# Performance work log

Measured on AMD Instinct MI355X. Metric: run time of the kernel, lower is better.

The kernel has to match this reference:

```python
import jax, jax.numpy as jnp
import numpy as np

B, N, C = 16, 4096, 512
H = 8                      # num_heads
HEIGHT = WIDTH = 64        # input_resolution, HEIGHT*WIDTH == N
D = C // H                 # head_dim = 64
SCALE = D ** (-0.25)       # head_dim ** -0.25 (applied to both axial logits)


def setup_inputs() -> dict:
    key = jax.random.key(0)
    k0, k1, k2 = jax.random.split(key, 3)
    return {
        "x": jax.random.normal(k0, (B, N, C), jnp.float32),
        "W_qkv": jax.random.normal(k1, (C, 3 * C), jnp.float32) / np.sqrt(C).astype(np.float32),
        "b_qkv": jnp.zeros((3 * C,), jnp.float32),
        "W_proj": jax.random.normal(k2, (C, C), jnp.float32) / np.sqrt(C).astype(np.float32),
        "b_proj": jnp.zeros((C,), jnp.float32),
    }


def reference(x, W_qkv, b_qkv, W_proj, b_proj):
    Bx, Nx, Cx = x.shape
    # qkv projection -> [3, B, H, height, width, D]
    qkv = (x @ W_qkv + b_qkv).reshape(Bx, Nx, 3, H, D)
    qkv = jnp.transpose(qkv, (2, 0, 3, 1, 4)).reshape(3, Bx, H, HEIGHT, WIDTH, D)
    q, k, v = qkv[0], qkv[1], qkv[2]

    # row attention (channel_merge='concat'): contract over (width, channel)
    a = jnp.einsum('bhiwc,bhjwc->bhij', q, k) * SCALE          # [B,H,height,height]
    a = jax.nn.softmax(a, axis=-1)
    # column attention: contract over (height, channel)
    bm = jnp.einsum('bhtic,bhtjc->bhij', q, k) * SCALE         # [B,H,width,width]
    bm = jax.nn.softmax(bm, axis=-1)

    # coupled combination: (v_perm @ b^T) then a @ (...)
    # tmp[b,h,c,t,u] = sum_w v[b,h,t,w,c] * bm[b,h,u,w]
    tmp = jnp.einsum('bhtwc,bhuw->bhctu', v, bm)               # [B,H,D,height,width]
    out = jnp.einsum('bhij,bhcjw->bhciw', a, tmp)              # [B,H,D,height,width]

    out = out.reshape(Bx, Cx, Nx).transpose(0, 2, 1)           # [B,N,C]
    return out @ W_proj + b_proj
```

## Files before the change

kernel.cpp:

```cpp
#include <hip/hip_runtime.h>
#include <math.h>

#define SCALE_F 0.35355339059327373f

typedef unsigned short u16;
typedef unsigned int   u32;
typedef _Float16 f16;
typedef _Float16 f16x8 __attribute__((ext_vector_type(8)));
typedef float    f32x4 __attribute__((ext_vector_type(4)));

__device__ __forceinline__ u16 f2h(float f) { f16 h = (f16)f; return *(u16*)&h; }
__device__ __forceinline__ float h2f(u16 b) { f16 h = *(f16*)&b; return (float)h; }

__device__ __forceinline__ void glds16(const u16* g, char* l) {
    __builtin_amdgcn_global_load_lds((const __attribute__((address_space(1))) void*)g,
                                     (__attribute__((address_space(3))) void*)l, 16, 0, 0);
}
__device__ __forceinline__ f32x4 mfma16(f16x8 a, f16x8 b, f32x4 c) {
    return __builtin_amdgcn_mfma_f32_16x16x32_f16(a, b, c, 0, 0, 0);
}

__global__ __launch_bounds__(256) void to_f16(
    const float* __restrict__ X, u16* __restrict__ out)
{
    size_t i = ((size_t)blockIdx.x * 256 + threadIdx.x) * 8;
    float4 a = *(const float4*)(X + i);
    float4 b = *(const float4*)(X + i + 4);
    ushort4 r0, r1;
    r0.x = f2h(a.x); r0.y = f2h(a.y); r0.z = f2h(a.z); r0.w = f2h(a.w);
    r1.x = f2h(b.x); r1.y = f2h(b.y); r1.z = f2h(b.z); r1.w = f2h(b.w);
    *(ushort4*)(out + i)     = r0;
    *(ushort4*)(out + i + 4) = r1;
}

__global__ __launch_bounds__(256) void transpose_f16(
    const float* __restrict__ in, u16* __restrict__ out, int R, int C)
{
    __shared__ __align__(16) u16 T[64 * 80];
    const int c0 = blockIdx.x * 64, r0 = blockIdx.y * 64, z = blockIdx.z;
    const int t = threadIdx.x;
    const int rl = t >> 4, c4 = (t & 15) * 4;
    const float* base = in + (size_t)z * R * C;

    #pragma unroll
    for (int rr = 0; rr < 4; ++rr) {
        int r = rr * 16 + rl;
        float4 v = *(const float4*)(base + (size_t)(r0 + r) * C + c0 + c4);
        T[(c4 + 0) * 80 + r] = f2h(v.x);
        T[(c4 + 1) * 80 + r] = f2h(v.y);
        T[(c4 + 2) * 80 + r] = f2h(v.z);
        T[(c4 + 3) * 80 + r] = f2h(v.w);
    }
    __syncthreads();
    #pragma unroll
    for (int rep = 0; rep < 2; ++rep) {
        int idx = rep * 256 + t;
        int cl = idx >> 3, r8 = (idx & 7) * 8;
        *(float4*)(out + ((size_t)z * C + c0 + cl) * R + r0 + r8) =
            *(const float4*)&T[cl * 80 + r8];
    }
}

__global__ __launch_bounds__(256) void transpose16(
    const u16* __restrict__ in, u16* __restrict__ out)
{
    __shared__ __align__(16) u16 T[64 * 80];
    const int c0 = blockIdx.x * 64, r0 = blockIdx.y * 64, z = blockIdx.z;
    const int t = threadIdx.x;
    const int rl = t >> 3;
    const int c8 = (t & 7) * 8;
    const u16* base = in + (size_t)z * 512 * 4096;

    #pragma unroll
    for (int rr = 0; rr < 2; ++rr) {
        int r = rr * 32 + rl;
        const u16* p = base + (size_t)(r0 + r) * 4096 + c0 + c8;
        ushort4 v0 = *(const ushort4*)(p);
        ushort4 v1 = *(const ushort4*)(p + 4);
        T[(c8 + 0) * 80 + r] = v0.x;
        T[(c8 + 1) * 80 + r] = v0.y;
        T[(c8 + 2) * 80 + r] = v0.z;
        T[(c8 + 3) * 80 + r] = v0.w;
        T[(c8 + 4) * 80 + r] = v1.x;
        T[(c8 + 5) * 80 + r] = v1.y;
        T[(c8 + 6) * 80 + r] = v1.z;
        T[(c8 + 7) * 80 + r] = v1.w;
    }
    __syncthreads();
    #pragma unroll
    for (int rep = 0; rep < 2; ++rep) {
        int idx = rep * 256 + t;
        int cl = idx >> 3, r8 = (idx & 7) * 8;
        *(float4*)(out + ((size_t)z * 4096 + c0 + cl) * 512 + r0 + r8) =
            *(const float4*)&T[cl * 80 + r8];
    }
}

__global__ __launch_bounds__(256) void qkv_mfma(
    const u16* __restrict__ Xh, const u16* __restrict__ WT,
    const float* __restrict__ bias,
    u16* __restrict__ Q, u16* __restrict__ Kk, u16* __restrict__ Vt)
{
    __shared__ __align__(16) char smem[33280];

    const int id  = blockIdx.x;
    const int xcd = id & 7;
    const int jj  = id >> 3;
    const int mt  = xcd * 64 + jj / 12;
    const int nt  = jj % 12;

    const int t = threadIdx.x;
    const int wave = t >> 6, lane = t & 63;
    const int wm = wave & 1, wn = wave >> 1;
    const int quad = lane >> 4, l16 = lane & 15;
    const int m0 = mt * 128;

    const int c0 = wave * 128 + lane;
    const int c1 = c0 + 64;
    const size_t xoff0 = (size_t)(m0 + (c0 & 127)) * 512 + (c0 >> 7) * 8;
    const size_t xoff1 = (size_t)(m0 + (c1 & 127)) * 512 + (c1 >> 7) * 8;
    const size_t woff0 = (size_t)(nt * 128 + (c0 & 127)) * 512 + (c0 >> 7) * 8;
    const size_t woff1 = (size_t)(nt * 128 + (c1 & 127)) * 512 + (c1 >> 7) * 8;
    const int lb0 = (wave * 128) * 16;
    const int lb1 = lb0 + 64 * 16;

    f32x4 acc[4][4];
    #pragma unroll
    for (int i = 0; i < 4; ++i)
        #pragma unroll
        for (int j = 0; j < 4; ++j) acc[i][j] = (f32x4){0.f, 0.f, 0.f, 0.f};

    glds16(Xh + xoff0, smem + lb0);
    glds16(Xh + xoff1, smem + lb1);
    glds16(WT + woff0, smem + 8192 + lb0);
    glds16(WT + woff1, smem + 8192 + lb1);
    __syncthreads();

    for (int k0 = 0; k0 < 512; k0 += 32) {
        const int co = (k0 & 32) << 9;
        const int cn = co ^ 16384;
        char* Ac = smem + co;
        char* Bc = smem + 8192 + co;
        if (k0 < 480) {
            glds16(Xh + xoff0 + k0 + 32, smem + cn + lb0);
            glds16(Xh + xoff1 + k0 + 32, smem + cn + lb1);
            glds16(WT + woff0 + k0 + 32, smem + 8192 + cn + lb0);
            glds16(WT + woff1 + k0 + 32, smem + 8192 + cn + lb1);
        }

        f16x8 af[4], bf[4];
        #pragma unroll
        for (int i = 0; i < 4; ++i)
            af[i] = *(const f16x8*)(Ac + (quad * 128 + wm * 64 + i * 16 + l16) * 16);
        #pragma unroll
        for (int j = 0; j < 4; ++j)
            bf[j] = *(const f16x8*)(Bc + (quad * 128 + wn * 64 + j * 16 + l16) * 16);
        #pragma unroll
        for (int i = 0; i < 4; ++i)
            #pragma unroll
            for (int j = 0; j < 4; ++j)
                acc[i][j] = mfma16(af[i], bf[j], acc[i][j]);

        __syncthreads();
    }

    const int b   = m0 >> 12;
    const int nn0 = m0 & 4095;
    float bv[4];
    #pragma unroll
    for (int j = 0; j < 4; ++j) bv[j] = bias[nt * 128 + wn * 64 + j * 16 + l16];

    if (nt < 8) {
        u16* dst = (nt < 4) ? Q : Kk;
        const int colbase = (nt & 3) * 128;
        #pragma unroll
        for (int i = 0; i < 4; ++i) {
            const int rowb = wm * 64 + i * 16 + quad * 4;
            #pragma unroll
            for (int j = 0; j < 4; ++j) {
                const int col = colbase + wn * 64 + j * 16 + l16;
                const int h = col >> 6, d = col & 63;
                u16* p = dst + ((size_t)((b * 8 + h) * 4096 + nn0 + rowb)) * 64 + d;
                #pragma unroll
                for (int r = 0; r < 4; ++r)
                    p[(size_t)r * 64] = f2h(acc[i][j][r] + bv[j]);
            }
        }
    } else {
        float* Tr = (float*)smem;
        #pragma unroll
        for (int g = 0; g < 2; ++g) {
            __syncthreads();
            if (wn == g) {
                #pragma unroll
                for (int i = 0; i < 4; ++i)
                    #pragma unroll
                    for (int j = 0; j < 4; ++j)
                        #pragma unroll
                        for (int r = 0; r < 4; ++r)
                            Tr[(wm * 64 + i * 16 + quad * 4 + r) * 65 + j * 16 + l16] =
                                acc[i][j][r] + bv[j];
            }
            __syncthreads();
            const int h = (nt & 3) * 2 + g;
            u16* dstv = Vt + ((size_t)(b * 8 + h) * 64) * 4096 + nn0;
            #pragma unroll
            for (int rep = 0; rep < 32; ++rep) {
                int idx = rep * 256 + t;
                int d = idx >> 7, rr = idx & 127;
                dstv[(size_t)d * 4096 + rr] = f2h(Tr[rr * 65 + d]);
            }
        }
    }
}

__global__ __launch_bounds__(256) void attn_logits(
    const u16* __restrict__ Q, const u16* __restrict__ Kk,
    float* __restrict__ Aout, float* __restrict__ Bmout)
{
    __shared__ float sm[64 * 68];
    __shared__ float red[128];

    const int bh   = blockIdx.x;
    const int mode = blockIdx.y;
    const int t    = threadIdx.x;
    const int wave = t >> 6, lane = t & 63;
    const int wr = wave & 1, wc = wave >> 1;
    const int quad = lane >> 4, l16 = lane & 15;

    const u16* Qb = Q  + (size_t)bh * 262144;
    const u16* Kb = Kk + (size_t)bh * 262144;

    const int rA0 = wr * 32 + l16, rA1 = rA0 + 16;
    const int rB0 = wc * 32 + l16, rB1 = rB0 + 16;

    f32x4 acc[2][2];
    #pragma unroll
    for (int i = 0; i < 2; ++i)
        #pragma unroll
        for (int j = 0; j < 2; ++j) acc[i][j] = (f32x4){0.f, 0.f, 0.f, 0.f};

    if (mode == 0) {
        const u16* pA0 = Qb + (size_t)rA0 * 4096;
        const u16* pA1 = Qb + (size_t)rA1 * 4096;
        const u16* pB0 = Kb + (size_t)rB0 * 4096;
        const u16* pB1 = Kb + (size_t)rB1 * 4096;
        #pragma unroll 4
        for (int k0 = 0; k0 < 4096; k0 += 32) {
            const int kk = k0 + quad * 8;
            f16x8 a0 = *(const f16x8*)(pA0 + kk);
            f16x8 a1 = *(const f16x8*)(pA1 + kk);
            f16x8 b0 = *(const f16x8*)(pB0 + kk);
            f16x8 b1 = *(const f16x8*)(pB1 + kk);
            acc[0][0] = mfma16(a0, b0, acc[0][0]);
            acc[0][1] = mfma16(a0, b1, acc[0][1]);
            acc[1][0] = mfma16(a1, b0, acc[1][0]);
            acc[1][1] = mfma16(a1, b1, acc[1][1]);
        }
    } else {
        #pragma unroll 4
        for (int k0 = 0; k0 < 4096; k0 += 32) {
            const int kk = k0 + quad * 8;
            const size_t base = (size_t)(kk >> 6) * 4096 + (kk & 63);
            f16x8 a0 = *(const f16x8*)(Qb + base + rA0 * 64);
            f16x8 a1 = *(const f16x8*)(Qb + base + rA1 * 64);
            f16x8 b0 = *(const f16x8*)(Kb + base + rB0 * 64);
            f16x8 b1 = *(const f16x8*)(Kb + base + rB1 * 64);
            acc[0][0] = mfma16(a0, b0, acc[0][0]);
            acc[0][1] = mfma16(a0, b1, acc[0][1]);
            acc[1][0] = mfma16(a1, b0, acc[1][0]);
            acc[1][1] = mfma16(a1, b1, acc[1][1]);
        }
    }

    #pragma unroll
    for (int i = 0; i < 2; ++i)
        #pragma unroll
        for (int j = 0; j < 2; ++j)
            #pragma unroll
            for (int r = 0; r < 4; ++r)
                sm[(wr * 32 + i * 16 + quad * 4 + r) * 68 + wc * 32 + j * 16 + l16] =
                    acc[i][j][r] * SCALE_F;
    __syncthreads();
    if (t < 64) {
        float m = -1e30f;
        for (int j = 0; j < 64; ++j) m = fmaxf(m, sm[t * 68 + j]);
        float ssum = 0.f;
        for (int j = 0; j < 64; ++j) ssum += __expf(sm[t * 68 + j] - m);
        red[t] = m;
        red[64 + t] = 1.0f / ssum;
    }
    __syncthreads();
    float* Out = ((mode == 0) ? Aout : Bmout) + (size_t)bh * 4096;
    #pragma unroll
    for (int rep = 0; rep < 16; ++rep) {
        int idx = rep * 256 + t;
        int i = idx >> 6, j = idx & 63;
        Out[idx] = __expf(sm[i * 68 + j] - red[i]) * red[64 + i];
    }
}

__global__ __launch_bounds__(256) void coupling(
    const u16* __restrict__ Vt, const float* __restrict__ Aatt,
    const float* __restrict__ Bm, u16* __restrict__ Yh)
{
    __shared__ __align__(16) u16 Ah[64 * 72];
    __shared__ __align__(16) u16 Bh[64 * 72];
    __shared__ __align__(16) u16 Tt[2][64 * 72];

    const int bh = blockIdx.x, cg = blockIdx.y;
    const int t = threadIdx.x;
    const int wave = t >> 6, lane = t & 63;
    const int wr = wave & 1, wc = wave >> 1;
    const int quad = lane >> 4, l16 = lane & 15;

    const float* Ab = Aatt + (size_t)bh * 4096;
    const float* Bb = Bm   + (size_t)bh * 4096;
    const u16*  Vb  = Vt   + (size_t)bh * 262144;
    u16* Yb = Yh + (size_t)bh * 262144;

    {
        const int row = t >> 2;
        const int colb = (t & 3) * 16;
        #pragma unroll
        for (int q = 0; q < 4; ++q) {
            float4 va = *(const float4*)(Ab + (size_t)row * 64 + colb + q * 4);
            Ah[row * 72 + colb + q * 4 + 0] = f2h(va.x);
            Ah[row * 72 + colb + q * 4 + 1] = f2h(va.y);
            Ah[row * 72 + colb + q * 4 + 2] = f2h(va.z);
            Ah[row * 72 + colb + q * 4 + 3] = f2h(va.w);
            float4 vb = *(const float4*)(Bb + (size_t)row * 64 + colb + q * 4);
            Bh[row * 72 + colb + q * 4 + 0] = f2h(vb.x);
            Bh[row * 72 + colb + q * 4 + 1] = f2h(vb.y);
            Bh[row * 72 + colb + q * 4 + 2] = f2h(vb.z);
            Bh[row * 72 + colb + q * 4 + 3] = f2h(vb.w);
        }
    }
    __syncthreads();

    for (int ci = 0; ci < 16; ++ci) {
        const int c = cg * 16 + ci;
        u16* tb = &Tt[ci & 1][0];

        f32x4 acc1[2][2];
        #pragma unroll
        for (int i = 0; i < 2; ++i)
            #pragma unroll
            for (int j = 0; j < 2; ++j) acc1[i][j] = (f32x4){0.f, 0.f, 0.f, 0.f};
        #pragma unroll
        for (int s = 0; s < 2; ++s) {
            f16x8 a1[2], b1[2];
            #pragma unroll
            for (int i = 0; i < 2; ++i)
                a1[i] = *(const f16x8*)&Bh[(wr * 32 + i * 16 + l16) * 72 + s * 32 + quad * 8];
            #pragma unroll
            for (int j = 0; j < 2; ++j)
                b1[j] = *(const f16x8*)(Vb + (size_t)c * 4096 +
                                        (size_t)(wc * 32 + j * 16 + l16) * 64 + s * 32 + quad * 8);
            #pragma unroll
            for (int i = 0; i < 2; ++i)
                #pragma unroll
                for (int j = 0; j < 2; ++j)
                    acc1[i][j] = mfma16(a1[i], b1[j], acc1[i][j]);
        }
        #pragma unroll
        for (int i = 0; i < 2; ++i)
            #pragma unroll
            for (int j = 0; j < 2; ++j)
                #pragma unroll
                for (int r = 0; r < 4; ++r)
                    tb[(wr * 32 + i * 16 + quad * 4 + r) * 72 + wc * 32 + j * 16 + l16] =
                        f2h(acc1[i][j][r]);
        __syncthreads();

        f32x4 acc2[2][2];
        #pragma unroll
        for (int i = 0; i < 2; ++i)
            #pragma unroll
            for (int j = 0; j < 2; ++j) acc2[i][j] = (f32x4){0.f, 0.f, 0.f, 0.f};
        #pragma unroll
        for (int s = 0; s < 2; ++s) {
            f16x8 a2[2], b2[2];
            #pragma unroll
            for (int i = 0; i < 2; ++i)
                a2[i] = *(const f16x8*)&Ah[(wr * 32 + i * 16 + l16) * 72 + s * 32 + quad * 8];
            #pragma unroll
            for (int u = 0; u < 2; ++u)
                b2[u] = *(const f16x8*)&tb[(wc * 32 + u * 16 + l16) * 72 + s * 32 + quad * 8];
            #pragma unroll
            for (int i = 0; i < 2; ++i)
                #pragma unroll
                for (int u = 0; u < 2; ++u)
                    acc2[i][u] = mfma16(a2[i], b2[u], acc2[i][u]);
        }
        #pragma unroll
        for (int i = 0; i < 2; ++i)
            #pragma unroll
            for (int u = 0; u < 2; ++u)
                #pragma unroll
                for (int r = 0; r < 4; ++r)
                    Yb[(size_t)c * 4096 + (wr * 32 + i * 16 + quad * 4 + r) * 64 +
                       wc * 32 + u * 16 + l16] = f2h(acc2[i][u][r]);
    }
}

__global__ __launch_bounds__(256) void proj_mfma(
    const u16* __restrict__ A, const u16* __restrict__ WT,
    const float* __restrict__ bias, float* __restrict__ Out)
{
    __shared__ __align__(16) char smem[32768];

    const int id  = blockIdx.x;
    const int xcd = id & 7;
    const int jj  = id >> 3;
    const int mt  = xcd * 64 + (jj >> 2);
    const int nt  = jj & 3;

    const int t = threadIdx.x;
    const int wave = t >> 6, lane = t & 63;
    const int wm = wave & 1, wn = wave >> 1;
    const int quad = lane >> 4, l16 = lane & 15;
    const int m0 = mt * 128;

    const int c0 = wave * 128 + lane;
    const int c1 = c0 + 64;
    const size_t aoff0 = (size_t)(m0 + (c0 & 127)) * 512 + (c0 >> 7) * 8;
    const size_t aoff1 = (size_t)(m0 + (c1 & 127)) * 512 + (c1 >> 7) * 8;
    const size_t woff0 = (size_t)(nt * 128 + (c0 & 127)) * 512 + (c0 >> 7) * 8;
    const size_t woff1 = (size_t)(nt * 128 + (c1 & 127)) * 512 + (c1 >> 7) * 8;
    const int lb0 = (wave * 128) * 16;
    const int lb1 = lb0 + 64 * 16;

    f32x4 acc[4][4];
    #pragma unroll
    for (int i = 0; i < 4; ++i)
        #pragma unroll
        for (int j = 0; j < 4; ++j) acc[i][j] = (f32x4){0.f, 0.f, 0.f, 0.f};

    glds16(A  + aoff0, smem + lb0);
    glds16(A  + aoff1, smem + lb1);
    glds16(WT + woff0, smem + 8192 + lb0);
    glds16(WT + woff1, smem + 8192 + lb1);
    __syncthreads();

    for (int k0 = 0; k0 < 512; k0 += 32) {
        const int co = (k0 & 32) << 9;
        const int cn = co ^ 16384;
        char* Ac = smem + co;
        char* Bc = smem + 8192 + co;
        if (k0 < 480) {
            glds16(A  + aoff0 + k0 + 32, smem + cn + lb0);
            glds16(A  + aoff1 + k0 + 32, smem + cn + lb1);
            glds16(WT + woff0 + k0 + 32, smem + 8192 + cn + lb0);
            glds16(WT + woff1 + k0 + 32, smem + 8192 + cn + lb1);
        }

        f16x8 af[4], bf[4];
        #pragma unroll
        for (int i = 0; i < 4; ++i)
            af[i] = *(const f16x8*)(Ac + (quad * 128 + wm * 64 + i * 16 + l16) * 16);
        #pragma unroll
        for (int j = 0; j < 4; ++j)
            bf[j] = *(const f16x8*)(Bc + (quad * 128 + wn * 64 + j * 16 + l16) * 16);
        #pragma unroll
        for (int i = 0; i < 4; ++i)
            #pragma unroll
            for (int j = 0; j < 4; ++j)
                acc[i][j] = mfma16(af[i], bf[j], acc[i][j]);

        __syncthreads();
    }

    float bv[4];
    #pragma unroll
    for (int j = 0; j < 4; ++j) bv[j] = bias[nt * 128 + wn * 64 + j * 16 + l16];

    #pragma unroll
    for (int i = 0; i < 4; ++i) {
        const int rowb = m0 + wm * 64 + i * 16 + quad * 4;
        #pragma unroll
        for (int j = 0; j < 4; ++j) {
            const int col = nt * 128 + wn * 64 + j * 16 + l16;
            #pragma unroll
            for (int r = 0; r < 4; ++r)
                Out[(size_t)(rowb + r) * 512 + col] = acc[i][j][r] + bv[j];
        }
    }
}

extern "C" void kernel_launch(void* const* d_in, const int* in_sizes, int n_in,
                              void* d_out, int out_size, void* d_ws, size_t ws_size,
                              hipStream_t stream)
{
    const float* x     = (const float*)d_in[0];
    const float* Wqkv  = (const float*)d_in[1];
    const float* bqkv  = (const float*)d_in[2];
    const float* Wproj = (const float*)d_in[3];
    const float* bproj = (const float*)d_in[4];
    float* out = (float*)d_out;

    u16* Xh  = (u16*)d_ws;
    u16* Qh  = Xh + 33554432;
    u16* Kh  = Qh + 33554432;
    u16* Vth = Kh + 33554432;
    u16* WqT = Vth + 33554432;
    u16* WpT = WqT + 786432;
    float* Aa = (float*)(WpT + 262144);
    float* Bm = Aa + 524288;
    u16* Yh  = Xh;
    u16* Ytb = Kh;

    to_f16        <<<16384, 256, 0, stream>>>(x, Xh);
    transpose_f16 <<<dim3(24, 8, 1),  256, 0, stream>>>(Wqkv,  WqT, 512, 1536);
    transpose_f16 <<<dim3(8, 8, 1),   256, 0, stream>>>(Wproj, WpT, 512, 512);
    qkv_mfma      <<<6144,            256, 0, stream>>>(Xh, WqT, bqkv, Qh, Kh, Vth);
    attn_logits   <<<dim3(128, 2),    256, 0, stream>>>(Qh, Kh, Aa, Bm);
    coupling      <<<dim3(128, 4),    256, 0, stream>>>(Vth, Aa, Bm, Yh);
    transpose16   <<<dim3(64, 8, 16), 256, 0, stream>>>(Yh, Ytb);
    proj_mfma     <<<2048,            256, 0, stream>>>(Ytb, WpT, bproj, out);
}
```

Measured before the change: 678.6 us.

## Enlarge QKV GEMM tiles to 256x256 with 512-thread blocks and vectorized V transpose

The QKV projection GEMM now uses 256x256 output tiles computed by 8 waves of 512 threads, each wave holding an 8x4 grid of MFMA accumulators. The aim is more operand reuse from LDS and less global reload traffic per FLOP. The V-transpose epilogue now stages fp16 values in LDS and writes 16-byte vector stores instead of scalar fp16 stores. In exchange it doubles LDS use to 64KB and raises register pressure, which may reduce occupancy.

```diff
diff --git a/kernel.cpp b/kernel.cpp
--- a/kernel.cpp
+++ b/kernel.cpp
@@ -96,67 +96,71 @@
     }
 }
 
-__global__ __launch_bounds__(256) void qkv_mfma(
+__global__ __launch_bounds__(512) void qkv_mfma(
     const u16* __restrict__ Xh, const u16* __restrict__ WT,
     const float* __restrict__ bias,
     u16* __restrict__ Q, u16* __restrict__ Kk, u16* __restrict__ Vt)
 {
-    __shared__ __align__(16) char smem[33280];
+    __shared__ __align__(16) char smem[65536];
 
     const int id  = blockIdx.x;
     const int xcd = id & 7;
     const int jj  = id >> 3;
-    const int mt  = xcd * 64 + jj / 12;
-    const int nt  = jj % 12;
+    const int mt  = xcd * 32 + jj / 6;
+    const int nt  = jj % 6;
 
     const int t = threadIdx.x;
     const int wave = t >> 6, lane = t & 63;
     const int wm = wave & 1, wn = wave >> 1;
     const int quad = lane >> 4, l16 = lane & 15;
-    const int m0 = mt * 128;
-
-    const int c0 = wave * 128 + lane;
-    const int c1 = c0 + 64;
-    const size_t xoff0 = (size_t)(m0 + (c0 & 127)) * 512 + (c0 >> 7) * 8;
-    const size_t xoff1 = (size_t)(m0 + (c1 & 127)) * 512 + (c1 >> 7) * 8;
-    const size_t woff0 = (size_t)(nt * 128 + (c0 & 127)) * 512 + (c0 >> 7) * 8;
-    const size_t woff1 = (size_t)(nt * 128 + (c1 & 127)) * 512 + (c1 >> 7) * 8;
-    const int lb0 = (wave * 128) * 16;
-    const int lb1 = lb0 + 64 * 16;
-
-    f32x4 acc[4][4];
-    #pragma unroll
-    for (int i = 0; i < 4; ++i)
+    const int m0 = mt * 256;
+
+    const int srow = (wave & 3) * 64 + lane;
+    size_t xoff[2], woff[2];
+    int lb[2];
+    #pragma unroll
+    for (int p = 0; p < 2; ++p) {
+        const int oct = p * 2 + (wave >> 2);
+        xoff[p] = (size_t)(m0 + srow) * 512 + oct * 8;
+        woff[p] = (size_t)(nt * 256 + srow) * 512 + oct * 8;
+        lb[p]   = (p * 512 + wave * 64) * 16;
+    }
+
+    f32x4 acc[8][4];
+    #pragma unroll
+    for (int i = 0; i < 8; ++i)
         #pragma unroll
         for (int j = 0; j < 4; ++j) acc[i][j] = (f32x4){0.f, 0.f, 0.f, 0.f};
 
-    glds16(Xh + xoff0, smem + lb0);
-    glds16(Xh + xoff1, smem + lb1);
-    glds16(WT + woff0, smem + 8192 + lb0);
-    glds16(WT + woff1, smem + 8192 + lb1);
+    #pragma unroll
+    for (int p = 0; p < 2; ++p) {
+        glds16(Xh + xoff[p], smem + lb[p]);
+        glds16(WT + woff[p], smem + 16384 + lb[p]);
+    }
     __syncthreads();
 
     for (int k0 = 0; k0 < 512; k0 += 32) {
-        const int co = (k0 & 32) << 9;
-        const int cn = co ^ 16384;
+        const int co = (k0 & 32) << 10;
+        const int cn = co ^ 32768;
         char* Ac = smem + co;
-        char* Bc = smem + 8192 + co;
+        char* Bc = smem + co + 16384;
         if (k0 < 480) {
-            glds16(Xh + xoff0 + k0 + 32, smem + cn + lb0);
-            glds16(Xh + xoff1 + k0 + 32, smem + cn + lb1);
-            glds16(WT + woff0 + k0 + 32, smem + 8192 + cn + lb0);
-            glds16(WT + woff1 + k0 + 32, smem + 8192 + cn + lb1);
-        }
-
-        f16x8 af[4], bf[4];
-        #pragma unroll
-        for (int i = 0; i < 4; ++i)
-            af[i] = *(const f16x8*)(Ac + (quad * 128 + wm * 64 + i * 16 + l16) * 16);
+            #pragma unroll
+            for (int p = 0; p < 2; ++p) {
+                glds16(Xh + xoff[p] + k0 + 32, smem + cn + lb[p]);
+                glds16(WT + woff[p] + k0 + 32, smem + cn + 16384 + lb[p]);
+            }
+        }
+
+        f16x8 af[8], bf[4];
+        #pragma unroll
+        for (int i = 0; i < 8; ++i)
+            af[i] = *(const f16x8*)(Ac + (quad * 256 + wm * 128 + i * 16 + l16) * 16);
         #pragma unroll
         for (int j = 0; j < 4; ++j)
-            bf[j] = *(const f16x8*)(Bc + (quad * 128 + wn * 64 + j * 16 + l16) * 16);
-        #pragma unroll
-        for (int i = 0; i < 4; ++i)
+            bf[j] = *(const f16x8*)(Bc + (quad * 256 + wn * 64 + j * 16 + l16) * 16);
+        #pragma unroll
+        for (int i = 0; i < 8; ++i)
             #pragma unroll
             for (int j = 0; j < 4; ++j)
                 acc[i][j] = mfma16(af[i], bf[j], acc[i][j]);
@@ -168,14 +172,14 @@
     const int nn0 = m0 & 4095;
     float bv[4];
     #pragma unroll
-    for (int j = 0; j < 4; ++j) bv[j] = bias[nt * 128 + wn * 64 + j * 16 + l16];
-
-    if (nt < 8) {
-        u16* dst = (nt < 4) ? Q : Kk;
-        const int colbase = (nt & 3) * 128;
-        #pragma unroll
-        for (int i = 0; i < 4; ++i) {
-            const int rowb = wm * 64 + i * 16 + quad * 4;
+    for (int j = 0; j < 4; ++j) bv[j] = bias[nt * 256 + wn * 64 + j * 16 + l16];
+
+    if (nt < 4) {
+        u16* dst = (nt < 2) ? Q : Kk;
+        const int colbase = (nt & 1) * 256;
+        #pragma unroll
+        for (int i = 0; i < 8; ++i) {
+            const int rowb = wm * 128 + i * 16 + quad * 4;
             #pragma unroll
             for (int j = 0; j < 4; ++j) {
                 const int col = colbase + wn * 64 + j * 16 + l16;
@@ -187,28 +191,30 @@
             }
         }
     } else {
-        float* Tr = (float*)smem;
-        #pragma unroll
-        for (int g = 0; g < 2; ++g) {
+        u16* Trt = (u16*)smem;
+        const int hb = (nt - 4) * 4;
+        #pragma unroll
+        for (int g = 0; g < 4; ++g) {
             __syncthreads();
             if (wn == g) {
                 #pragma unroll
-                for (int i = 0; i < 4; ++i)
+                for (int i = 0; i < 8; ++i)
                     #pragma unroll
                     for (int j = 0; j < 4; ++j)
                         #pragma unroll
                         for (int r = 0; r < 4; ++r)
-                            Tr[(wm * 64 + i * 16 + quad * 4 + r) * 65 + j * 16 + l16] =
-                                acc[i][j][r] + bv[j];
+                            Trt[(j * 16 + l16) * 272 + wm * 128 + i * 16 + quad * 4 + r] =
+                                f2h(acc[i][j][r] + bv[j]);
             }
             __syncthreads();
-            const int h = (nt & 3) * 2 + g;
+            const int h = hb + g;
             u16* dstv = Vt + ((size_t)(b * 8 + h) * 64) * 4096 + nn0;
             #pragma unroll
-            for (int rep = 0; rep < 32; ++rep) {
-                int idx = rep * 256 + t;
-                int d = idx >> 7, rr = idx & 127;
-                dstv[(size_t)d * 4096 + rr] = f2h(Tr[rr * 65 + d]);
+            for (int rep = 0; rep < 4; ++rep) {
+                int idx = rep * 512 + t;
+                int d = idx >> 5, r8 = (idx & 31) * 8;
+                *(float4*)(dstv + (size_t)d * 4096 + r8) =
+                    *(const float4*)&Trt[d * 272 + r8];
             }
         }
     }
@@ -513,7 +519,7 @@
     to_f16        <<<16384, 256, 0, stream>>>(x, Xh);
     transpose_f16 <<<dim3(24, 8, 1),  256, 0, stream>>>(Wqkv,  WqT, 512, 1536);
     transpose_f16 <<<dim3(8, 8, 1),   256, 0, stream>>>(Wproj, WpT, 512, 512);
-    qkv_mfma      <<<6144,            256, 0, stream>>>(Xh, WqT, bqkv, Qh, Kh, Vth);
+    qkv_mfma      <<<1536,            512, 0, stream>>>(Xh, WqT, bqkv, Qh, Kh, Vth);
     attn_logits   <<<dim3(128, 2),    256, 0, stream>>>(Qh, Kh, Aa, Bm);
     coupling      <<<dim3(128, 4),    256, 0, stream>>>(Vth, Aa, Bm, Yh);
     transpose16   <<<dim3(64, 8, 16), 256, 0, stream>>>(Yh, Ytb);
```

Result: faster. 663.5 us (-2.2%).
